# Performance work log

Hardware: AMD Instinct MI355X
Metric: run time of the kernel (lower is better)

Reference implementation:

```python
import jax, jax.numpy as jnp
import numpy as np

HEADS = 16
DIM = 1024
HEAD_DIM = DIM // HEADS


def setup_inputs() -> dict:
    key = jax.random.key(0)
    k1, k2 = jax.random.split(key)
    images = jax.random.normal(k1, (2, 2048, DIM), dtype=jnp.float32)
    # torch nn.Linear(dim, 3*dim, bias=False): y = x @ W.T, W: [3*dim, dim].
    # Store as [dim, 3*dim] for direct x @ W_qkv.
    W_qkv = jax.random.normal(k2, (DIM, 3 * DIM), dtype=jnp.float32) / np.sqrt(DIM)
    return {"images": images, "W_qkv": W_qkv}


def reference(images, W_qkv):
    B, S, D = images.shape
    qkv = images @ W_qkv  # [B, S, 3D]
    q, k, v = jnp.split(qkv, 3, axis=-1)
    # [B, S, H, Dh] -> [B, H, S, Dh]
    def to_heads(t):
        return t.reshape(B, S, HEADS, HEAD_DIM).transpose(0, 2, 1, 3)
    q, k, v = to_heads(q), to_heads(k), to_heads(v)
    scale = 1.0 / jnp.sqrt(jnp.asarray(HEAD_DIM, dtype=q.dtype))
    scores = jnp.einsum('bhqd,bhkd->bhqk', q, k) * scale  # [B, H, S, S]
    probs = jax.nn.softmax(scores, axis=-1)
    out = jnp.einsum('bhqk,bhkd->bhqd', probs, v)  # [B, H, S, Dh]
    return out.transpose(0, 2, 1, 3).reshape(B, S, D)
```

## Files before the change

### kernel.cpp

```cpp
#include <hip/hip_runtime.h>
#include <hip/hip_bf16.h>
#include <math.h>

typedef __bf16 bf16x8 __attribute__((ext_vector_type(8)));
typedef float f32x4 __attribute__((ext_vector_type(4)));
typedef unsigned short u16x8 __attribute__((ext_vector_type(8)));
typedef unsigned short u16;

#define S_LEN 2048
#define DMODEL 1024
#define NH 16

__device__ __forceinline__ u16 f2bf(float f) {
    __bf16 b = (__bf16)f;
    return __builtin_bit_cast(u16, b);
}
__device__ __forceinline__ float bf2f(u16 u) {
    union { unsigned int i; float f; } v; v.i = ((unsigned int)u) << 16; return v.f;
}

__device__ __forceinline__ void gload16(const u16* g, u16* lds_base) {
    __builtin_amdgcn_global_load_lds(
        (const __attribute__((address_space(1))) unsigned int*)g,
        (__attribute__((address_space(3))) unsigned int*)lds_base,
        16, 0, 0);
}

__global__ __launch_bounds__(256) void cvt_x(const float* __restrict__ in, u16* __restrict__ outp) {
    int i = (blockIdx.x * 256 + threadIdx.x) * 4;
    float4 v = *(const float4*)(in + i);
    outp[i + 0] = f2bf(v.x); outp[i + 1] = f2bf(v.y);
    outp[i + 2] = f2bf(v.z); outp[i + 3] = f2bf(v.w);
}

__global__ __launch_bounds__(256) void transpose_w(const float* __restrict__ W, u16* __restrict__ Wt) {
    __shared__ u16 tile[32][33];
    int n0 = blockIdx.x * 32, k0 = blockIdx.y * 32;
    int tx = threadIdx.x & 31, ty = threadIdx.x >> 5;
#pragma unroll
    for (int i = 0; i < 4; i++) {
        int k = ty + i * 8;
        tile[k][tx] = f2bf(W[(size_t)(k0 + k) * 3072 + n0 + tx]);
    }
    __syncthreads();
#pragma unroll
    for (int i = 0; i < 4; i++) {
        int n = ty + i * 8;
        Wt[(size_t)(n0 + n) * 1024 + k0 + tx] = tile[tx][n];
    }
}

__global__ __launch_bounds__(256) void qkv_gemm(const u16* __restrict__ A, const u16* __restrict__ Bt,
                                                u16* __restrict__ C) {
    __shared__ alignas(16) u16 As[128 * 64];
    __shared__ alignas(16) u16 Bs[128 * 64];
    const int tid = threadIdx.x, l = tid & 63, w = tid >> 6;
    const int bm = blockIdx.y, bn = blockIdx.x;
    const int wm = w >> 1, wn = w & 1;
    const int c0 = l & 15, g = l >> 4;
    f32x4 acc[4][4] = {};
    for (int kt = 0; kt < 1024; kt += 64) {
        __syncthreads();
#pragma unroll
        for (int n = 0; n < 4; n++) {
            int i = tid + n * 256;
            int r = i >> 3, c = i & 7;
            int cs = c ^ (r & 7);
            u16* dstA = As + (size_t)(w * 64 + n * 256) * 8;
            u16* dstB = Bs + (size_t)(w * 64 + n * 256) * 8;
            gload16(A + (size_t)(bm * 128 + r) * 1024 + kt + cs * 8, dstA);
            gload16(Bt + (size_t)(bn * 128 + r) * 1024 + kt + cs * 8, dstB);
        }
        __syncthreads();
#pragma unroll
        for (int kk = 0; kk < 2; kk++) {
            bf16x8 af[4], bfr[4];
#pragma unroll
            for (int m = 0; m < 4; m++) {
                int row = wm * 64 + m * 16 + c0;
                af[m] = *(const bf16x8*)((const char*)As + row * 128 + (((g + kk * 4) ^ (row & 7)) << 4));
            }
#pragma unroll
            for (int n = 0; n < 4; n++) {
                int row = wn * 64 + n * 16 + c0;
                bfr[n] = *(const bf16x8*)((const char*)Bs + row * 128 + (((g + kk * 4) ^ (row & 7)) << 4));
            }
#pragma unroll
            for (int m = 0; m < 4; m++)
#pragma unroll
                for (int n = 0; n < 4; n++)
                    acc[m][n] = __builtin_amdgcn_mfma_f32_16x16x32_bf16(af[m], bfr[n], acc[m][n], 0, 0, 0);
        }
    }
#pragma unroll
    for (int m = 0; m < 4; m++)
#pragma unroll
        for (int n = 0; n < 4; n++)
#pragma unroll
            for (int j = 0; j < 4; j++) {
                int row = bm * 128 + wm * 64 + m * 16 + 4 * g + j;
                int col = bn * 128 + wn * 64 + n * 16 + c0;
                C[(size_t)row * 3072 + col] = f2bf(acc[m][n][j]);
            }
}

__global__ __launch_bounds__(256) void transpose_v(const u16* __restrict__ QKV, u16* __restrict__ Vtp) {
    __shared__ u16 tile[64][72];
    const int bh = blockIdx.x >> 5, st = blockIdx.x & 31;
    const int b = bh >> 4, h = bh & 15;
    const u16* src = QKV + (size_t)b * S_LEN * 3072 + 2048 + h * 64;
    const int sl = threadIdx.x >> 2;
    const int cg = (threadIdx.x & 3) * 16;
#pragma unroll
    for (int ii = 0; ii < 2; ii++) {
        u16x8 v = *(const u16x8*)(src + (size_t)(st * 64 + sl) * 3072 + cg + ii * 8);
        *(u16x8*)&tile[sl][cg + ii * 8] = v;
    }
    __syncthreads();
    const int dl = threadIdx.x >> 2;
#pragma unroll
    for (int ii = 0; ii < 2; ii++) {
        u16x8 o;
#pragma unroll
        for (int q = 0; q < 8; q++) {
            int p = cg + ii * 8 + q;
            int kb = 2 * (p >> 5) + ((p >> 2) & 1);
            int t = kb * 16 + ((p >> 3) & 3) * 4 + (p & 3);
            o[q] = tile[t][dl];
        }
        *(u16x8*)(Vtp + ((size_t)bh * 64 + dl) * S_LEN + st * 64 + cg + ii * 8) = o;
    }
}

__global__ __launch_bounds__(512, 4) void attn11(const u16* __restrict__ QKV, const u16* __restrict__ Vtp,
                                                 float* __restrict__ outp) {
    __shared__ alignas(16) u16 Ks[2][2][64 * 64];
    __shared__ alignas(16) u16 Vs[2][2][64 * 64];
    const int bid = blockIdx.x;
    const int wg = ((bid & 7) << 7) | (bid >> 3);
    const int tid = threadIdx.x, l = tid & 63, w = tid >> 6;
    const int hf = w >> 2, wsub = w & 3;
    const int qt = wg & 31, bh = wg >> 5;
    const int b = bh >> 4, h = bh & 15;
    const int c0 = l & 15, g = l >> 4;
    const u16* Qb = QKV + (size_t)b * S_LEN * 3072 + h * 64;
    const u16* Kb = Qb + 1024;
    const u16* Vb = Vtp + (size_t)bh * 64 * S_LEN;
    const int kv0 = hf * 1024;
    const int qrow = qt * 64 + wsub * 16 + c0;

    const int tid_h = tid & 255;
    const int r0 = tid_h >> 3, cs0 = (tid_h & 7) ^ (r0 & 7);
    const int i1 = tid_h + 256, r1 = i1 >> 3, cs1 = (i1 & 7) ^ (r1 & 7);
    const int dbA = (wsub * 64) * 8, dbB = (256 + wsub * 64) * 8;

    int off[8];
#pragma unroll
    for (int x = 0; x < 4; x++)
#pragma unroll
        for (int kk = 0; kk < 2; kk++)
            off[x * 2 + kk] = (x * 16 + c0) * 128 + (((g + 4 * kk) ^ (c0 & 7)) << 4);

    bf16x8 qf[2];
    {
        const float qs = 0.125f * 1.44269504f;
#pragma unroll
        for (int kk = 0; kk < 2; kk++) {
            u16x8 v = *(const u16x8*)(Qb + (size_t)qrow * 3072 + kk * 32 + g * 8);
            bf16x8 q;
#pragma unroll
            for (int j = 0; j < 8; j++) q[j] = (__bf16)(bf2f(v[j]) * qs);
            qf[kk] = q;
        }
    }
    bf16x8 vone;
#pragma unroll
    for (int j = 0; j < 8; j++) vone[j] = (__bf16)1.0f;

    float m_r = 0.f;
    f32x4 accO[4] = {};
    f32x4 accL = {};

    gload16(Kb + (size_t)(kv0 + r0) * 3072 + cs0 * 8, Ks[hf][0] + dbA);
    gload16(Kb + (size_t)(kv0 + r1) * 3072 + cs1 * 8, Ks[hf][0] + dbB);
    gload16(Vb + (size_t)r0 * S_LEN + kv0 + cs0 * 8, Vs[hf][0] + dbA);
    gload16(Vb + (size_t)r1 * S_LEN + kv0 + cs1 * 8, Vs[hf][0] + dbB);

    for (int t = 0; t < 16; t++) {
        const int cur = t & 1;
        __syncthreads();
        if (t + 1 < 16) {
            const int kvn = kv0 + (t + 1) * 64;
            gload16(Kb + (size_t)(kvn + r0) * 3072 + cs0 * 8, Ks[hf][cur ^ 1] + dbA);
            gload16(Kb + (size_t)(kvn + r1) * 3072 + cs1 * 8, Ks[hf][cur ^ 1] + dbB);
            gload16(Vb + (size_t)r0 * S_LEN + kvn + cs0 * 8, Vs[hf][cur ^ 1] + dbA);
            gload16(Vb + (size_t)r1 * S_LEN + kvn + cs1 * 8, Vs[hf][cur ^ 1] + dbB);
        }
        const char* Kc = (const char*)Ks[hf][cur];
        const char* Vc = (const char*)Vs[hf][cur];
        f32x4 sc[4];
        const float nm = -m_r;
#pragma unroll
        for (int kb = 0; kb < 4; kb++) { sc[kb][0] = nm; sc[kb][1] = nm; sc[kb][2] = nm; sc[kb][3] = nm; }
        __builtin_amdgcn_s_setprio(1);
#pragma unroll
        for (int kb = 0; kb < 4; kb++)
#pragma unroll
            for (int kk = 0; kk < 2; kk++) {
                bf16x8 kf = *(const bf16x8*)(Kc + off[kb * 2 + kk]);
                sc[kb] = __builtin_amdgcn_mfma_f32_16x16x32_bf16(kf, qf[kk], sc[kb], 0, 0, 0);
            }
        __builtin_amdgcn_s_setprio(0);
        bf16x8 vf[2][4];
#pragma unroll
        for (int kk = 0; kk < 2; kk++)
#pragma unroll
            for (int n = 0; n < 4; n++)
                vf[kk][n] = *(const bf16x8*)(Vc + off[n * 2 + kk]);
        float m0 = fmaxf(fmaxf(sc[0][0], sc[0][1]), sc[0][2]);
        float m1 = fmaxf(fmaxf(sc[0][3], sc[1][0]), sc[1][1]);
        float m2 = fmaxf(fmaxf(sc[1][2], sc[1][3]), sc[2][0]);
        float m3 = fmaxf(fmaxf(sc[2][1], sc[2][2]), sc[2][3]);
        float m4 = fmaxf(fmaxf(sc[3][0], sc[3][1]), sc[3][2]);
        float mx = fmaxf(fmaxf(fmaxf(m0, m1), m2), fmaxf(fmaxf(m3, m4), sc[3][3]));
        if (!__all(mx <= 8.f)) {
            float mxr = fmaxf(mx, __shfl_xor(mx, 16));
            mxr = fmaxf(mxr, __shfl_xor(mxr, 32));
            float adj = fmaxf(mxr, 0.f);
            float alpha = __builtin_amdgcn_exp2f(-adj);
            m_r += adj;
#pragma unroll
            for (int j = 0; j < 4; j++) {
                float aj = __shfl(alpha, 20 * g + j);
                accL[j] *= aj;
#pragma unroll
                for (int n = 0; n < 4; n++) accO[n][j] *= aj;
            }
#pragma unroll
            for (int kb = 0; kb < 4; kb++)
#pragma unroll
                for (int j = 0; j < 4; j++) sc[kb][j] -= adj;
        }
#pragma unroll
        for (int kb = 0; kb < 4; kb++)
#pragma unroll
            for (int j = 0; j < 4; j++)
                sc[kb][j] = __builtin_amdgcn_exp2f(sc[kb][j]);
        __builtin_amdgcn_s_setprio(1);
#pragma unroll
        for (int kk = 0; kk < 2; kk++) {
            bf16x8 pf;
#pragma unroll
            for (int j = 0; j < 4; j++) {
                pf[j]     = (__bf16)sc[2 * kk][j];
                pf[j + 4] = (__bf16)sc[2 * kk + 1][j];
            }
            accL = __builtin_amdgcn_mfma_f32_16x16x32_bf16(pf, vone, accL, 0, 0, 0);
#pragma unroll
            for (int n = 0; n < 4; n++)
                accO[n] = __builtin_amdgcn_mfma_f32_16x16x32_bf16(pf, vf[kk][n], accO[n], 0, 0, 0);
        }
        __builtin_amdgcn_s_setprio(0);
    }
    __syncthreads();
    float* Opart = (float*)&Ks[0][0][0];
    float* m1s   = (float*)&Vs[0][0][0];
    float* l1s   = m1s + 64;
    if (hf == 1) {
#pragma unroll
        for (int j = 0; j < 4; j++) {
            int rj = wsub * 16 + 4 * g + j;
#pragma unroll
            for (int n = 0; n < 4; n++) Opart[rj * 65 + n * 16 + c0] = accO[n][j];
        }
        if (g == 0) m1s[wsub * 16 + c0] = m_r;
        if (c0 == 0) {
#pragma unroll
            for (int j = 0; j < 4; j++) l1s[wsub * 16 + 4 * g + j] = accL[j];
        }
    }
    __syncthreads();
    if (hf == 0) {
#pragma unroll
        for (int j = 0; j < 4; j++) {
            int rj = wsub * 16 + 4 * g + j;
            float m1v = m1s[rj], l1v = l1s[rj];
            float m0v = __shfl(m_r, 20 * g + j);
            float M = fmaxf(m0v, m1v);
            float a0 = __builtin_amdgcn_exp2f(m0v - M);
            float a1 = __builtin_amdgcn_exp2f(m1v - M);
            float inv = 1.0f / (a0 * accL[j] + a1 * l1v);
            float* op = outp + ((size_t)b * S_LEN + qt * 64 + rj) * DMODEL + h * 64;
#pragma unroll
            for (int n = 0; n < 4; n++)
                op[n * 16 + c0] = (a0 * accO[n][j] + a1 * Opart[rj * 65 + n * 16 + c0]) * inv;
        }
    }
}

extern "C" void kernel_launch(void* const* d_in, const int* in_sizes, int n_in,
                              void* d_out, int out_size, void* d_ws, size_t ws_size,
                              hipStream_t stream) {
    const float* X = (const float*)d_in[0];
    const float* W = (const float*)d_in[1];
    float* out = (float*)d_out;

    u16* Xb  = (u16*)d_ws;
    u16* Wt  = Xb + (size_t)4096 * 1024;
    u16* QKV = Wt + (size_t)3072 * 1024;
    u16* Vtp = QKV + (size_t)4096 * 3072;

    cvt_x<<<4096, 256, 0, stream>>>(X, Xb);
    transpose_w<<<dim3(96, 32), 256, 0, stream>>>(W, Wt);
    qkv_gemm<<<dim3(24, 32), 256, 0, stream>>>(Xb, Wt, QKV);
    transpose_v<<<1024, 256, 0, stream>>>(QKV, Vtp);
    attn11<<<1024, 512, 0, stream>>>(QKV, Vtp, out);
}
```

Before: 107.2 us.

## Merge input prep kernels and fuse V transpose into QKV GEMM epilogue

Combines the X conversion and W transpose into one prep launch split by block index. The V-head transpose moves into the QKV GEMM epilogue, so blocks covering V columns write directly in the permuted Vtp layout instead of storing V and re-reading it in a separate kernel. This removes two launches and one round-trip of V through global memory. The cost is 8-byte scattered stores in the GEMM epilogue for V blocks.

```diff
diff --git a/kernel.cpp b/kernel.cpp
--- a/kernel.cpp
+++ b/kernel.cpp
@@ -5,6 +5,7 @@
 typedef __bf16 bf16x8 __attribute__((ext_vector_type(8)));
 typedef float f32x4 __attribute__((ext_vector_type(4)));
 typedef unsigned short u16x8 __attribute__((ext_vector_type(8)));
+typedef unsigned short u16x4 __attribute__((ext_vector_type(4)));
 typedef unsigned short u16;
 
 #define S_LEN 2048
@@ -26,32 +27,35 @@
         16, 0, 0);
 }
 
-__global__ __launch_bounds__(256) void cvt_x(const float* __restrict__ in, u16* __restrict__ outp) {
-    int i = (blockIdx.x * 256 + threadIdx.x) * 4;
-    float4 v = *(const float4*)(in + i);
-    outp[i + 0] = f2bf(v.x); outp[i + 1] = f2bf(v.y);
-    outp[i + 2] = f2bf(v.z); outp[i + 3] = f2bf(v.w);
-}
-
-__global__ __launch_bounds__(256) void transpose_w(const float* __restrict__ W, u16* __restrict__ Wt) {
+__global__ __launch_bounds__(256) void prep(const float* __restrict__ X, u16* __restrict__ Xb,
+                                            const float* __restrict__ W, u16* __restrict__ Wt) {
     __shared__ u16 tile[32][33];
-    int n0 = blockIdx.x * 32, k0 = blockIdx.y * 32;
-    int tx = threadIdx.x & 31, ty = threadIdx.x >> 5;
-#pragma unroll
-    for (int i = 0; i < 4; i++) {
-        int k = ty + i * 8;
-        tile[k][tx] = f2bf(W[(size_t)(k0 + k) * 3072 + n0 + tx]);
-    }
-    __syncthreads();
-#pragma unroll
-    for (int i = 0; i < 4; i++) {
-        int n = ty + i * 8;
-        Wt[(size_t)(n0 + n) * 1024 + k0 + tx] = tile[tx][n];
+    const int bid = blockIdx.x;
+    if (bid < 4096) {
+        int i = (bid * 256 + threadIdx.x) * 4;
+        float4 v = *(const float4*)(X + i);
+        Xb[i + 0] = f2bf(v.x); Xb[i + 1] = f2bf(v.y);
+        Xb[i + 2] = f2bf(v.z); Xb[i + 3] = f2bf(v.w);
+    } else {
+        int bid2 = bid - 4096;
+        int n0 = (bid2 % 96) * 32, k0 = (bid2 / 96) * 32;
+        int tx = threadIdx.x & 31, ty = threadIdx.x >> 5;
+#pragma unroll
+        for (int i = 0; i < 4; i++) {
+            int k = ty + i * 8;
+            tile[k][tx] = f2bf(W[(size_t)(k0 + k) * 3072 + n0 + tx]);
+        }
+        __syncthreads();
+#pragma unroll
+        for (int i = 0; i < 4; i++) {
+            int n = ty + i * 8;
+            Wt[(size_t)(n0 + n) * 1024 + k0 + tx] = tile[tx][n];
+        }
     }
 }
 
 __global__ __launch_bounds__(256) void qkv_gemm(const u16* __restrict__ A, const u16* __restrict__ Bt,
-                                                u16* __restrict__ C) {
+                                                u16* __restrict__ C, u16* __restrict__ Vtp) {
     __shared__ alignas(16) u16 As[128 * 64];
     __shared__ alignas(16) u16 Bs[128 * 64];
     const int tid = threadIdx.x, l = tid & 63, w = tid >> 6;
@@ -92,43 +96,34 @@
                     acc[m][n] = __builtin_amdgcn_mfma_f32_16x16x32_bf16(af[m], bfr[n], acc[m][n], 0, 0, 0);
         }
     }
-#pragma unroll
-    for (int m = 0; m < 4; m++)
-#pragma unroll
-        for (int n = 0; n < 4; n++)
-#pragma unroll
-            for (int j = 0; j < 4; j++) {
-                int row = bm * 128 + wm * 64 + m * 16 + 4 * g + j;
-                int col = bn * 128 + wn * 64 + n * 16 + c0;
-                C[(size_t)row * 3072 + col] = f2bf(acc[m][n][j]);
-            }
-}
-
-__global__ __launch_bounds__(256) void transpose_v(const u16* __restrict__ QKV, u16* __restrict__ Vtp) {
-    __shared__ u16 tile[64][72];
-    const int bh = blockIdx.x >> 5, st = blockIdx.x & 31;
-    const int b = bh >> 4, h = bh & 15;
-    const u16* src = QKV + (size_t)b * S_LEN * 3072 + 2048 + h * 64;
-    const int sl = threadIdx.x >> 2;
-    const int cg = (threadIdx.x & 3) * 16;
-#pragma unroll
-    for (int ii = 0; ii < 2; ii++) {
-        u16x8 v = *(const u16x8*)(src + (size_t)(st * 64 + sl) * 3072 + cg + ii * 8);
-        *(u16x8*)&tile[sl][cg + ii * 8] = v;
-    }
-    __syncthreads();
-    const int dl = threadIdx.x >> 2;
-#pragma unroll
-    for (int ii = 0; ii < 2; ii++) {
-        u16x8 o;
-#pragma unroll
-        for (int q = 0; q < 8; q++) {
-            int p = cg + ii * 8 + q;
-            int kb = 2 * (p >> 5) + ((p >> 2) & 1);
-            int t = kb * 16 + ((p >> 3) & 3) * 4 + (p & 3);
-            o[q] = tile[t][dl];
-        }
-        *(u16x8*)(Vtp + ((size_t)bh * 64 + dl) * S_LEN + st * 64 + cg + ii * 8) = o;
+    if (bn < 16) {
+#pragma unroll
+        for (int m = 0; m < 4; m++)
+#pragma unroll
+            for (int n = 0; n < 4; n++)
+#pragma unroll
+                for (int j = 0; j < 4; j++) {
+                    int row = bm * 128 + wm * 64 + m * 16 + 4 * g + j;
+                    int col = bn * 128 + wn * 64 + n * 16 + c0;
+                    C[(size_t)row * 3072 + col] = f2bf(acc[m][n][j]);
+                }
+    } else {
+        const int h = (bn - 16) * 2 + wn;
+#pragma unroll
+        for (int m = 0; m < 4; m++) {
+            int srow_g = bm * 128 + wm * 64 + m * 16 + 4 * g;
+            int b = srow_g >> 11;
+            int srow = srow_g & 2047;
+            int sbase = (srow & ~63) + 32 * (m >> 1) + 8 * g + 4 * (m & 1);
+#pragma unroll
+            for (int n = 0; n < 4; n++) {
+                int d = n * 16 + c0;
+                u16x4 v;
+#pragma unroll
+                for (int j = 0; j < 4; j++) v[j] = f2bf(acc[m][n][j]);
+                *(u16x4*)(Vtp + ((size_t)(b * 16 + h) * 64 + d) * S_LEN + sbase) = v;
+            }
+        }
     }
 }
 
@@ -310,9 +305,7 @@
     u16* QKV = Wt + (size_t)3072 * 1024;
     u16* Vtp = QKV + (size_t)4096 * 3072;
 
-    cvt_x<<<4096, 256, 0, stream>>>(X, Xb);
-    transpose_w<<<dim3(96, 32), 256, 0, stream>>>(W, Wt);
-    qkv_gemm<<<dim3(24, 32), 256, 0, stream>>>(Xb, Wt, QKV);
-    transpose_v<<<1024, 256, 0, stream>>>(QKV, Vtp);
+    prep<<<7168, 256, 0, stream>>>(X, Xb, W, Wt);
+    qkv_gemm<<<dim3(24, 32), 256, 0, stream>>>(Xb, Wt, QKV, Vtp);
     attn11<<<1024, 512, 0, stream>>>(QKV, Vtp, out);
 }
```

Result: faster. 101.0 us (-5.8%).
